# Kernel tuning notes

Hardware: AMD Instinct MI355X
Metric: run time of the kernel (lower is better)

The kernel has to match this reference:

```python
import jax, jax.numpy as jnp
import numpy as np
from jax import lax

ANCHORS = jnp.array([[-83.0, -39.0, 100.0, 56.0], [-175.0, -87.0, 192.0, 104.0],
                     [-359.0, -183.0, 376.0, 200.0], [-55.0, -55.0, 72.0, 72.0],
                     [-119.0, -119.0, 136.0, 136.0], [-247.0, -247.0, 264.0, 264.0],
                     [-35.0, -79.0, 52.0, 96.0], [-79.0, -167.0, 96.0, 184.0],
                     [-167.0, -343.0, 184.0, 360.0]], dtype=jnp.float32)
FEAT_STRIDE = 16
NMS_THRESH = 0.7
NA = 9
PRE_NMS_TOPN = 3000   # test_pre_nms_topN
POST_NMS_TOPN = 300   # test_post_nms_topN


def setup_inputs() -> dict:
    key = jax.random.key(0)
    ks = jax.random.split(key, 4)
    B, C, H, W = 8, 512, 64, 64
    x = jax.random.normal(ks[0], (B, C, H, W), jnp.float32)
    im_size = jnp.full((B, 2), 1024.0, jnp.float32)  # (H, W) per image
    W_conv = jax.random.normal(ks[1], (512, C, 3, 3), jnp.float32) * 0.01
    b_conv = jnp.zeros((512,), jnp.float32)
    W_reg = jax.random.normal(ks[2], (36, 512), jnp.float32) * 0.01
    b_reg = jnp.zeros((36,), jnp.float32)
    W_cls = jax.random.normal(ks[3], (18, 512), jnp.float32) * 0.01
    b_cls = jnp.zeros((18,), jnp.float32)
    return {"x": x, "im_size": im_size, "W_conv": W_conv, "b_conv": b_conv,
            "W_reg": W_reg, "b_reg": b_reg, "W_cls": W_cls, "b_cls": b_cls}


def _nms_select(boxes):
    """Greedy NMS on boxes already sorted by descending score.
    Returns [POST_NMS_TOPN, 4], zero-padded (matches torch output init)."""
    M = boxes.shape[0]
    area = (boxes[:, 2] - boxes[:, 0]) * (boxes[:, 3] - boxes[:, 1])
    lt = jnp.maximum(boxes[:, None, :2], boxes[None, :, :2])
    rb = jnp.minimum(boxes[:, None, 2:], boxes[None, :, 2:])
    wh = jnp.maximum(rb - lt, 0.0)
    inter = wh[..., 0] * wh[..., 1]
    iou = inter / (area[:, None] + area[None, :] - inter + 1e-9)
    iou = lax.stop_gradient(iou)
    idxs = jnp.arange(M)

    def body(keep, i):
        sup = (iou[i] > NMS_THRESH) & (idxs > i) & keep[i]
        return keep & ~sup, None

    keep, _ = lax.scan(body, jnp.ones((M,), bool), idxs)
    key = jnp.where(keep, idxs, M)           # push suppressed to the end
    order = jnp.sort(key)[:POST_NMS_TOPN]
    valid = order < M
    gi = jnp.minimum(order, M - 1)
    return jnp.where(valid[:, None], boxes[gi], 0.0)


def reference(x, im_size, W_conv, b_conv, W_reg, b_reg, W_cls, b_cls):
    B = x.shape[0]
    conv = lax.conv_general_dilated(
        x, W_conv, window_strides=(1, 1), padding='SAME',
        dimension_numbers=('NCHW', 'OIHW', 'NCHW')) + b_conv[None, :, None, None]
    Hc, Wc = conv.shape[2], conv.shape[3]

    # bbox deltas from raw (pre-ReLU) conv features, as in the source
    reg = jnp.einsum('bchw,oc->bohw', conv, W_reg) + b_reg[None, :, None, None]
    delta = reg.transpose(0, 2, 3, 1).reshape(B, -1, 4)  # (B, H*W*9, 4)

    # scores from ReLU'd features; channel-pair softmax trick, take class 0
    feat = jax.nn.relu(conv)
    cls = jnp.einsum('bchw,oc->bohw', feat, W_cls) + b_cls[None, :, None, None]
    c2 = cls.reshape(B, 2, NA * Hc, Wc)
    scores = jax.nn.softmax(c2, axis=1)[:, 0].reshape(B, -1)  # (B, 9*H*W)

    # anchor shifting: (h, w, anchor) ordering matches delta layout
    sx = jnp.arange(Wc, dtype=x.dtype) * FEAT_STRIDE
    sy = jnp.arange(Hc, dtype=x.dtype) * FEAT_STRIDE
    gx, gy = jnp.meshgrid(sx, sy)  # (Hc, Wc) 'xy' indexing
    shifts = jnp.stack([gx.ravel(), gy.ravel(), gx.ravel(), gy.ravel()], axis=1)
    anc = (shifts[:, None, :] + ANCHORS[None, :, :]).reshape(-1, 4)  # (H*W*9, 4)

    # decode, faithful to the source's (nonstandard) math
    w = anc[:, 2] - anc[:, 0] + 1.0
    h = anc[:, 3] - anc[:, 1] + 1.0
    cx = anc[:, 0] + 0.5 * w
    cy = anc[:, 1] + 0.5 * h
    dx, dy, dw, dh = delta[..., 0], delta[..., 1], delta[..., 2], delta[..., 3]
    pcx = dx * cx
    pcy = dy * cy
    pw = jnp.exp(dw) * w
    ph = jnp.exp(dh) * h
    x1, y1 = pcx - 0.5 * pw, pcy - 0.5 * ph
    x2, y2 = pcx + 0.5 * pw, pcy + 0.5 * ph

    # clip to image bounds (im_size[i] = (H, W))
    xmax = im_size[:, 1:2] - 1.0  # (B,1)
    ymax = im_size[:, 0:1] - 1.0
    x1 = jnp.clip(x1, 0.0, xmax)
    y1 = jnp.clip(y1, 0.0, ymax)
    x2 = jnp.clip(x2, 0.0, xmax)
    y2 = jnp.clip(y2, 0.0, ymax)
    proposals = jnp.stack([x1, y1, x2, y2], axis=-1)  # (B, N, 4)

    # pre-NMS top-k by score, then greedy NMS, keep post_nms_topN
    _, top_i = lax.top_k(scores, PRE_NMS_TOPN)
    top_b = jnp.take_along_axis(proposals, top_i[..., None], axis=1)
    output = jax.vmap(_nms_select)(top_b)  # (B, POST_NMS_TOPN, 4)

    return output, scores, proposals
```

## Files before the change

### kernel.cpp

```cpp
#include <hip/hip_runtime.h>
#include <stdint.h>

typedef unsigned long long u64;
typedef double v4d __attribute__((ext_vector_type(4)));

#define NIMG 8
#define CIN 512
#define COUT 512
#define NPOS 4096
#define NSC 36864
#define PRE_TOPN 3000
#define POST_TOPN 300
#define NWORDS 47
#define MSTRIDE 48
#define WROWF 80
#define WCH_F 5760
#define WBUF_B 23040
#define XBUF 1920
#define XVALID 1632

__constant__ double dANC[9][4] = {
    {-83.0, -39.0, 100.0, 56.0},   {-175.0, -87.0, 192.0, 104.0},
    {-359.0, -183.0, 376.0, 200.0},{-55.0, -55.0, 72.0, 72.0},
    {-119.0, -119.0, 136.0, 136.0},{-247.0, -247.0, 264.0, 264.0},
    {-35.0, -79.0, 52.0, 96.0},    {-79.0, -167.0, 96.0, 184.0},
    {-167.0, -343.0, 184.0, 360.0}};

static __device__ __forceinline__ void gload16(const void* g, void* l) {
    __builtin_amdgcn_global_load_lds(
        (const __attribute__((address_space(1))) void*)g,
        (__attribute__((address_space(3))) void*)l, 16, 0, 0);
}

__global__ __launch_bounds__(256) void transpose_wconv_f32(const float* __restrict__ W,
                                                           float* __restrict__ Wtf) {
    __shared__ float t[32][33];
    int k0 = blockIdx.x * 32;
    int o0 = blockIdx.y * 32;
    int tid = threadIdx.x;
    for (int idx = tid; idx < 1024; idx += 256) {
        int r = idx >> 5, c = idx & 31;
        t[r][c] = W[(size_t)(o0 + r) * 4608 + k0 + c];
    }
    __syncthreads();
    for (int idx = tid; idx < 1024; idx += 256) {
        int r = idx >> 5, c = idx & 31;
        int oc = o0 + c;
        Wtf[((size_t)(oc >> 6) * 4608 + (k0 + r)) * WROWF + (oc & 63)] = t[c][r];
    }
}

__global__ __launch_bounds__(256) void build_wheads(const float* __restrict__ Wreg,
                                                    const float* __restrict__ Wcls,
                                                    float* __restrict__ Wh) {
    int g = blockIdx.x * 256 + threadIdx.x;
    if (g >= 512 * 64) return;
    int k = g >> 6, o = g & 63;
    float v = 0.f;
    if (o < 36) v = Wreg[o * 512 + k];
    else if (o < 54) v = Wcls[(o - 36) * 512 + k];
    Wh[g] = v;
}

__global__ __launch_bounds__(64) void mfma_probe(int* __restrict__ variant) {
    __shared__ double AA[72][16];
    __shared__ double BB[72][16];
    const int L = threadIdx.x;
    for (int i = L; i < 72 * 16; i += 64) {
        int K = i >> 4, c = i & 15;
        AA[K][c] = (double)(c * 73 + K + 1);
        BB[K][c] = (double)(K * 17 + 3 * c + 1);
    }
    __syncthreads();
    const int lg = L >> 4, lm = L & 15;
    v4d accN = {0.0, 0.0, 0.0, 0.0};
    v4d accS = {0.0, 0.0, 0.0, 0.0};
#pragma unroll
    for (int k4 = 0; k4 < 18; ++k4) {
        double a = AA[4 * k4 + lg][lm];
        double b = BB[4 * k4 + lg][lm];
        accN = __builtin_amdgcn_mfma_f64_16x16x4f64(a, b, accN, 0, 0, 0);
        accS = __builtin_amdgcn_mfma_f64_16x16x4f64(b, a, accS, 0, 0, 0);
    }
    int found = 255;
    for (int v = 0; v < 8; ++v) {
        bool ok = true;
        for (int r = 0; r < 4; ++r) {
            int m, n;
            int dm = v & 3;
            if (dm == 0)      { m = 4 * lg + r; n = lm; }
            else if (dm == 1) { m = lm; n = 4 * lg + r; }
            else if (dm == 2) { m = lg + 4 * r; n = lm; }
            else              { m = lm; n = lg + 4 * r; }
            long long ref = 0;
            for (int K = 0; K < 72; ++K)
                ref += (long long)(m * 73 + K + 1) * (long long)(K * 17 + 3 * n + 1);
            double got = (v < 4) ? accN[r] : accS[r];
            ok = ok && (got == (double)ref);
        }
        if (__all(ok) && found == 255) found = v;
    }
    if (L == 0) *variant = found;
}

__global__ __launch_bounds__(512) void conv_mfma(const float* __restrict__ X,
                                                 const float* __restrict__ Wtf,
                                                 const float* __restrict__ bconv,
                                                 double* __restrict__ convb,
                                                 const int* __restrict__ variant,
                                                 int img_base) {
    const int vr = *variant;
    if (vr > 7) return;
    const int tid = threadIdx.x;
    const int wv = tid >> 6;
    const int lane = tid & 63;
    const int lg = lane >> 4;
    const int lm = lane & 15;
    const int ocg = wv >> 1;
    const int posb = (wv & 1) * 32;
    const int octile = blockIdx.x;
    const int oc0 = octile * 64;
    const int y = blockIdx.y;
    const int imgL = blockIdx.z;
    const int img_g = img_base + imgL;

    __shared__ float Wl[2][72][WROWF];
    __shared__ float Xl[2][8][3][80];
    char* wl0 = (char*)&Wl[0][0][0];
    float* xl0 = &Xl[0][0][0][0];

    v4d acc[2];
    acc[0] = (v4d){0.0, 0.0, 0.0, 0.0};
    acc[1] = (v4d){0.0, 0.0, 0.0, 0.0};

    int boff[18];
#pragma unroll
    for (int k4 = 0; k4 < 18; ++k4) {
        int row = k4 * 4 + lg;
        int c = row / 9;
        int t = row - 9 * c;
        int ty = t / 3;
        int tx = t - 3 * ty;
        boff[k4] = c * 240 + ty * 80 + tx + posb + lm;
    }

    int xli[4], xoff[4];
#pragma unroll
    for (int i = 0; i < 4; ++i) {
        int idx = tid + i * 512;
        xli[i] = -1;
        xoff[i] = -1;
        if (idx < XVALID) {
            int c_l = idx / 204;
            int rem = idx - c_l * 204;
            int r = rem / 68;
            int xx = rem - r * 68;
            xli[i] = c_l * 240 + r * 80 + xx;
            int yy = y + r - 1;
            int xg = xx - 1;
            if (xx < 66 && (unsigned)yy < 64u && (unsigned)xg < 64u)
                xoff[i] = ((img_g * CIN + c_l) * 64 + yy) * 64 + xg;
        }
    }
    int woff[3];
#pragma unroll
    for (int i = 0; i < 3; ++i) {
        int u = i * 512 + tid;
        int row = u / 20, cp = u - 20 * row;
        woff[i] = (octile * 4608 + row) * WROWF + cp * 4;
    }

    float xr[4];

#define WDMA(c, par) { \
    gload16(&Wtf[(size_t)woff[0] + (size_t)(c) * WCH_F], \
            wl0 + (size_t)(par) * WBUF_B + (size_t)tid * 16); \
    gload16(&Wtf[(size_t)woff[1] + (size_t)(c) * WCH_F], \
            wl0 + (size_t)(par) * WBUF_B + (size_t)(512 + tid) * 16); \
    if (tid < 416) \
        gload16(&Wtf[(size_t)woff[2] + (size_t)(c) * WCH_F], \
                wl0 + (size_t)(par) * WBUF_B + (size_t)(1024 + tid) * 16); }

#define LOADR(c) { \
    _Pragma("unroll") \
    for (int i = 0; i < 4; ++i) \
        xr[i] = (xoff[i] >= 0) ? X[(size_t)xoff[i] + (size_t)(c) * 32768] : 0.f; }

#define WRITER(par) { \
    _Pragma("unroll") \
    for (int i = 0; i < 4; ++i) \
        if (xli[i] >= 0) xl0[(size_t)(par) * XBUF + xli[i]] = xr[i]; }

    WDMA(0, 0);
    LOADR(0);
    WRITER(0);
    __syncthreads();

    const bool swapped = (vr >= 4);
    const int aoff = ocg * 16 + lm;

    for (int c = 0; c < 64; ++c) {
        const int par = c & 1;
        if (c < 63) { WDMA(c + 1, par ^ 1); LOADR(c + 1); }
        const float* wb = &Wl[par][0][0];
        const float* bx = xl0 + (size_t)par * XBUF;
        if (!swapped) {
#pragma unroll
            for (int k4 = 0; k4 < 18; ++k4) {
                double a = (double)wb[(4 * k4 + lg) * WROWF + aoff];
                const float* bp = bx + boff[k4];
                double b0 = (double)bp[0];
                double b1 = (double)bp[16];
                acc[0] = __builtin_amdgcn_mfma_f64_16x16x4f64(a, b0, acc[0], 0, 0, 0);
                acc[1] = __builtin_amdgcn_mfma_f64_16x16x4f64(a, b1, acc[1], 0, 0, 0);
            }
        } else {
#pragma unroll
            for (int k4 = 0; k4 < 18; ++k4) {
                double a = (double)wb[(4 * k4 + lg) * WROWF + aoff];
                const float* bp = bx + boff[k4];
                double b0 = (double)bp[0];
                double b1 = (double)bp[16];
                acc[0] = __builtin_amdgcn_mfma_f64_16x16x4f64(b0, a, acc[0], 0, 0, 0);
                acc[1] = __builtin_amdgcn_mfma_f64_16x16x4f64(b1, a, acc[1], 0, 0, 0);
            }
        }
        if (c < 63) { WRITER(par ^ 1); }
        __syncthreads();
    }
#undef WDMA
#undef LOADR
#undef WRITER

    const int dm = vr & 3;
#pragma unroll
    for (int q = 0; q < 2; ++q) {
#pragma unroll
        for (int r = 0; r < 4; ++r) {
            int m, n;
            if (dm == 0)      { m = 4 * lg + r; n = lm; }
            else if (dm == 1) { m = lm; n = 4 * lg + r; }
            else if (dm == 2) { m = lg + 4 * r; n = lm; }
            else              { m = lm; n = lg + 4 * r; }
            int oc = oc0 + ocg * 16 + m;
            int xp = posb + q * 16 + n;
            convb[((size_t)imgL * COUT + oc) * NPOS + y * 64 + xp] =
                acc[q][r] + (double)bconv[oc];
        }
    }
}

__global__ __launch_bounds__(256) void conv_valu(const float* __restrict__ X,
                                                 const float* __restrict__ Wtf,
                                                 const float* __restrict__ bconv,
                                                 double* __restrict__ convb,
                                                 const int* __restrict__ variant,
                                                 int img_base) {
    if (*variant <= 7) return;
    const int tid = threadIdx.x;
    const int octile = blockIdx.x;
    const int oc0 = octile * 64;
    const int y = blockIdx.y;
    const int imgL = blockIdx.z;
    const int img_g = img_base + imgL;
    const int x_l = (tid & 15) * 4;
    const int oc_l = (tid >> 4) * 4;

    __shared__ double Wl[72][64];
    __shared__ double Bx[8][3][68];

    double acc[4][4];
#pragma unroll
    for (int i = 0; i < 4; ++i)
#pragma unroll
        for (int j = 0; j < 4; ++j) acc[i][j] = 0.0;

    for (int cc = 0; cc < CIN; cc += 8) {
        __syncthreads();
        for (int idx = tid; idx < 8 * 3 * 68; idx += 256) {
            int c_l = idx / 204;
            int rem = idx - c_l * 204;
            int r = rem / 68;
            int xx = rem - r * 68;
            int yy = y + r - 1;
            int xg = xx - 1;
            float v = 0.f;
            if (xx < 66 && (unsigned)yy < 64u && (unsigned)xg < 64u)
                v = X[(((size_t)img_g * CIN + cc + c_l) * 64 + yy) * 64 + xg];
            Bx[c_l][r][xx] = (double)v;
        }
        for (int idx = tid; idx < 72 * 64; idx += 256) {
            int kl = idx >> 6, col = idx & 63;
            Wl[kl][col] = (double)Wtf[((size_t)octile * 4608 + cc * 9 + kl) * WROWF + col];
        }
        __syncthreads();
#pragma unroll 2
        for (int c_l = 0; c_l < 8; ++c_l) {
#pragma unroll
            for (int ty = 0; ty < 3; ++ty) {
                double xv[6];
                *(double2*)&xv[0] = *(const double2*)&Bx[c_l][ty][x_l + 0];
                *(double2*)&xv[2] = *(const double2*)&Bx[c_l][ty][x_l + 2];
                *(double2*)&xv[4] = *(const double2*)&Bx[c_l][ty][x_l + 4];
#pragma unroll
                for (int tx = 0; tx < 3; ++tx) {
                    const double* wp = &Wl[c_l * 9 + ty * 3 + tx][oc_l];
                    double wr[4];
                    *(double2*)&wr[0] = *(const double2*)(wp + 0);
                    *(double2*)&wr[2] = *(const double2*)(wp + 2);
#pragma unroll
                    for (int i = 0; i < 4; ++i)
#pragma unroll
                        for (int j = 0; j < 4; ++j)
                            acc[i][j] = fma(wr[i], xv[j + tx], acc[i][j]);
                }
            }
        }
    }
#pragma unroll
    for (int i = 0; i < 4; ++i) {
        int oc = oc0 + oc_l + i;
        double b = (double)bconv[oc];
        double4 st;
        st.x = acc[i][0] + b; st.y = acc[i][1] + b;
        st.z = acc[i][2] + b; st.w = acc[i][3] + b;
        *(double4*)&convb[((size_t)imgL * COUT + oc) * NPOS + y * 64 + x_l] = st;
    }
}

__global__ __launch_bounds__(256) void heads_kernel(const double* __restrict__ convb,
                                                    const float* __restrict__ Wh,
                                                    const float* __restrict__ breg,
                                                    const float* __restrict__ bcls,
                                                    const float* __restrict__ im_size,
                                                    float* __restrict__ out_scores,
                                                    float4* __restrict__ out_props,
                                                    double* __restrict__ dscores,
                                                    double4* __restrict__ dprops,
                                                    int img_base) {
    const int tid = threadIdx.x;
    const int y = blockIdx.x;
    const int imgL = blockIdx.y;
    const int img_g = img_base + imgL;

    __shared__ double cl[64][64];
    __shared__ float wl[64][64];

    const int o = tid & 63;
    const int g = tid >> 6;
    double acc[16];
#pragma unroll
    for (int j = 0; j < 16; ++j) acc[j] = 0.0;

    for (int k0 = 0; k0 < CIN; k0 += 64) {
        __syncthreads();
        for (int idx = tid; idx < 4096; idx += 256) {
            int kl = idx >> 6, p = idx & 63;
            cl[kl][p] = convb[((size_t)imgL * COUT + k0 + kl) * NPOS + y * 64 + p];
        }
        for (int idx = tid; idx < 4096; idx += 256) {
            wl[idx >> 6][idx & 63] = Wh[(k0 + (idx >> 6)) * 64 + (idx & 63)];
        }
        __syncthreads();
        const bool ru = (o >= 36);
        for (int kl = 0; kl < 64; ++kl) {
            double w = (double)wl[kl][o];
#pragma unroll
            for (int j = 0; j < 16; ++j) {
                double v = cl[kl][g * 16 + j];
                if (ru) v = fmax(v, 0.0);
                acc[j] = fma(w, v, acc[j]);
            }
        }
    }
    __syncthreads();
    double bias = (o < 36) ? (double)breg[o] : (o < 54 ? (double)bcls[o - 36] : 0.0);
#pragma unroll
    for (int j = 0; j < 16; ++j) cl[o][g * 16 + j] = acc[j] + bias;
    __syncthreads();

    const double im_h = (double)im_size[img_g * 2 + 0];
    const double im_w = (double)im_size[img_g * 2 + 1];
    const double xmax = im_w - 1.0, ymax = im_h - 1.0;

    for (int t = tid; t < 576; t += 256) {
        int p = t / 9;
        int a = t - p * 9;
        double dx = cl[a * 4 + 0][p], dy = cl[a * 4 + 1][p];
        double dw = cl[a * 4 + 2][p], dh = cl[a * 4 + 3][p];
        double c0 = cl[36 + a][p], c1 = cl[45 + a][p];
        double mm = fmax(c0, c1);
        double e0 = exp(c0 - mm), e1 = exp(c1 - mm);
        double sc = e0 / (e0 + e1);

        double sx = (double)p * 16.0, sy = (double)y * 16.0;
        double a0 = dANC[a][0] + sx, a1 = dANC[a][1] + sy;
        double a2 = dANC[a][2] + sx, a3 = dANC[a][3] + sy;
        double w_ = a2 - a0 + 1.0, h_ = a3 - a1 + 1.0;
        double cx = a0 + 0.5 * w_, cy = a1 + 0.5 * h_;
        double pcx = dx * cx, pcy = dy * cy;
        double pw = exp(dw) * w_, ph = exp(dh) * h_;
        double x1 = pcx - 0.5 * pw, y1 = pcy - 0.5 * ph;
        double x2 = pcx + 0.5 * pw, y2 = pcy + 0.5 * ph;
        x1 = fmin(fmax(x1, 0.0), xmax);
        y1 = fmin(fmax(y1, 0.0), ymax);
        x2 = fmin(fmax(x2, 0.0), xmax);
        y2 = fmin(fmax(y2, 0.0), ymax);

        int pp = y * 64 + p;
        size_t si = (size_t)img_g * NSC + (size_t)a * NPOS + pp;
        size_t pi = (size_t)img_g * NSC + (size_t)pp * 9 + a;
        out_scores[si] = (float)sc;
        dscores[si] = sc;
        double4 db; db.x = x1; db.y = y1; db.z = x2; db.w = y2;
        dprops[pi] = db;
        out_props[pi] = make_float4((float)x1, (float)y1, (float)x2, (float)y2);
    }
}

__global__ __launch_bounds__(256) void topk_select(const double* __restrict__ dscores,
                                                   u64* __restrict__ Tsel) {
    const int img = blockIdx.x;
    const int tid = threadIdx.x;
    const u64* sb = (const u64*)(dscores + (size_t)img * NSC);
    __shared__ uint32_t hist[256];
    __shared__ u64 s_prefix;
    __shared__ uint32_t s_rem;
    if (tid == 0) { s_prefix = 0ull; s_rem = PRE_TOPN; }
    for (int pass = 0; pass < 8; ++pass) {
        int shift = 56 - pass * 8;
        hist[tid] = 0;
        __syncthreads();
        u64 pmask = pass ? (~0ull << (shift + 8)) : 0ull;
        u64 pref = s_prefix;
        for (int i = tid; i < NSC; i += 256) {
            u64 v = sb[i];
            if ((v & pmask) == pref) atomicAdd(&hist[(uint32_t)(v >> shift) & 0xFFu], 1u);
        }
        __syncthreads();
        if (tid == 0) {
            uint32_t rem = s_rem, cum = 0;
            int b = 255;
            for (; b > 0; --b) {
                if (cum + hist[b] >= rem) break;
                cum += hist[b];
            }
            s_prefix = pref | ((u64)(uint32_t)b << shift);
            s_rem = rem - cum;
        }
        __syncthreads();
    }
    if (tid == 0) Tsel[img] = s_prefix;
}

__global__ __launch_bounds__(1024) void sort_gather(const double* __restrict__ dscores,
                                                    const double4* __restrict__ dprops,
                                                    const u64* __restrict__ Tsel,
                                                    double4* __restrict__ dboxes) {
    const int img = blockIdx.x;
    const int tid = threadIdx.x;
    __shared__ u64 skey[4096];
    __shared__ unsigned short sidx[4096];
    __shared__ int cnt;
    if (tid == 0) cnt = 0;
    for (int i = tid; i < 4096; i += 1024) { skey[i] = 0ull; sidx[i] = 0xFFFF; }
    __syncthreads();
    const u64 T = Tsel[img];
    const u64* sb = (const u64*)(dscores + (size_t)img * NSC);
    for (int i = tid; i < NSC; i += 1024) {
        u64 v = sb[i];
        if (v >= T) {
            int p = atomicAdd(&cnt, 1);
            if (p < 4096) { skey[p] = v; sidx[p] = (unsigned short)i; }
        }
    }
    __syncthreads();
    for (int k = 2; k <= 4096; k <<= 1) {
        for (int j = k >> 1; j > 0; j >>= 1) {
            for (int i = tid; i < 4096; i += 1024) {
                int ixj = i ^ j;
                if (ixj > i) {
                    u64 ka = skey[i], kb = skey[ixj];
                    unsigned short ia = sidx[i], ib = sidx[ixj];
                    bool aw = (ka < kb) || (ka == kb && ia > ib);
                    bool up = (i & k) == 0;
                    if (up ? aw : !aw) {
                        skey[i] = kb; skey[ixj] = ka;
                        sidx[i] = ib; sidx[ixj] = ia;
                    }
                }
            }
            __syncthreads();
        }
    }
    for (int t = tid; t < PRE_TOPN; t += 1024) {
        unsigned int idx = sidx[t];
        dboxes[(size_t)img * PRE_TOPN + t] = dprops[(size_t)img * NSC + idx];
    }
}

__global__ __launch_bounds__(256) void iou_mask_kernel(const double4* __restrict__ dboxes,
                                                       u64* __restrict__ mask) {
    const int tid = threadIdx.x;
    const int ib = blockIdx.x;
    const int img = blockIdx.y;
    const int i = ib * 64 + (tid >> 2);
    if (i >= PRE_TOPN) return;
    const double4 bi = dboxes[(size_t)img * PRE_TOPN + i];
    const double ai = (bi.z - bi.x) * (bi.w - bi.y);
    for (int w = (tid & 3); w < NWORDS; w += 4) {
        const int jbase = w * 64;
        u64 m = 0;
        if (jbase + 63 > i) {
            const int jmax = min(64, PRE_TOPN - jbase);
            for (int b = 0; b < jmax; ++b) {
                int j = jbase + b;
                if (j > i) {
                    double4 bj = dboxes[(size_t)img * PRE_TOPN + j];
                    double aj = (bj.z - bj.x) * (bj.w - bj.y);
                    double ltx = fmax(bi.x, bj.x), lty = fmax(bi.y, bj.y);
                    double rbx = fmin(bi.z, bj.z), rby = fmin(bi.w, bj.w);
                    double iw = fmax(rbx - ltx, 0.0), ih = fmax(rby - lty, 0.0);
                    double inter = iw * ih;
                    double iou = inter / (ai + aj - inter + 1e-9);
                    if (iou > 0.7) m |= (1ull << b);
                }
            }
        }
        mask[((size_t)img * PRE_TOPN + i) * MSTRIDE + w] = m;
    }
}

__global__ __launch_bounds__(64) void nms_walk(const double4* __restrict__ dboxes,
                                               const u64* __restrict__ mask,
                                               float4* __restrict__ outb) {
    const int img = blockIdx.x;
    const int lane = threadIdx.x;
    __shared__ short kept[POST_TOPN];
    u64 removed = 0ull;
    int nk = 0;
    for (int w = 0; w < NWORDS && nk < POST_TOPN; ++w) {
        u64 freeb = ~__shfl(removed, w);
        if (w == NWORDS - 1)
            freeb &= (1ull << (PRE_TOPN - (NWORDS - 1) * 64)) - 1;
        while (freeb != 0ull && nk < POST_TOPN) {
            int b = __ffsll((unsigned long long)freeb) - 1;
            int i = w * 64 + b;
            if (lane == 0) kept[nk] = (short)i;
            ++nk;
            u64 m = (lane < NWORDS)
                        ? mask[((size_t)img * PRE_TOPN + i) * MSTRIDE + lane]
                        : 0ull;
            removed |= m;
            u64 hi = (b == 63) ? 0ull : (~0ull << (b + 1));
            freeb &= hi;
            freeb &= ~__shfl(removed, w);
        }
    }
    __syncthreads();
    const int n = nk;
    for (int r = lane; r < POST_TOPN; r += 64) {
        float4 v = make_float4(0.f, 0.f, 0.f, 0.f);
        if (r < n) {
            double4 d = dboxes[(size_t)img * PRE_TOPN + kept[r]];
            v = make_float4((float)d.x, (float)d.y, (float)d.z, (float)d.w);
        }
        outb[img * POST_TOPN + r] = v;
    }
}

extern "C" void kernel_launch(void* const* d_in, const int* in_sizes, int n_in,
                              void* d_out, int out_size, void* d_ws, size_t ws_size,
                              hipStream_t stream) {
    const float* x = (const float*)d_in[0];
    const float* im_size = (const float*)d_in[1];
    const float* Wconv = (const float*)d_in[2];
    const float* bconv = (const float*)d_in[3];
    const float* Wreg = (const float*)d_in[4];
    const float* breg = (const float*)d_in[5];
    const float* Wcls = (const float*)d_in[6];
    const float* bcls = (const float*)d_in[7];

    float* outf = (float*)d_out;
    float4* out_boxes = (float4*)outf;
    float* out_scores = outf + NIMG * POST_TOPN * 4;
    float4* out_props = (float4*)(out_scores + (size_t)NIMG * NSC);

    char* ws = (char*)d_ws;
    const size_t WT_OFF = 0;
    const size_t WH_OFF = WT_OFF + (size_t)8 * 4608 * WROWF * 4;
    const size_t TS_OFF = WH_OFF + (size_t)512 * 64 * 4;
    const size_t VAR_OFF = TS_OFF + 64;
    const size_t DS_OFF = (VAR_OFF + 4 + 255) & ~(size_t)255;
    const size_t DP_OFF = DS_OFF + (size_t)NIMG * NSC * 8;
    const size_t DB_OFF = DP_OFF + (size_t)NIMG * NSC * 32;
    const size_t MK_OFF = DB_OFF + (size_t)NIMG * PRE_TOPN * 32;
    const size_t CV_OFF = (MK_OFF + (size_t)NIMG * PRE_TOPN * MSTRIDE * 8 + 255) & ~(size_t)255;

    float* Wtf = (float*)(ws + WT_OFF);
    float* Wh = (float*)(ws + WH_OFF);
    u64* Tsel = (u64*)(ws + TS_OFF);
    int* variant = (int*)(ws + VAR_OFF);
    double* dscores = (double*)(ws + DS_OFF);
    double4* dprops = (double4*)(ws + DP_OFF);
    double4* dboxes = (double4*)(ws + DB_OFF);
    u64* mask = (u64*)(ws + MK_OFF);
    double* convb = (double*)(ws + CV_OFF);

    const size_t per_img = (size_t)COUT * NPOS * 8;
    int CH = 1;
    if (ws_size > CV_OFF + per_img) {
        size_t avail = (ws_size - CV_OFF) / per_img;
        CH = (int)(avail > 8 ? 8 : avail);
        if (CH < 1) CH = 1;
    }

    transpose_wconv_f32<<<dim3(144, 16), 256, 0, stream>>>(Wconv, Wtf);
    build_wheads<<<128, 256, 0, stream>>>(Wreg, Wcls, Wh);
    mfma_probe<<<1, 64, 0, stream>>>(variant);

    for (int base = 0; base < NIMG; base += CH) {
        int n = NIMG - base;
        if (n > CH) n = CH;
        conv_mfma<<<dim3(8, 64, n), 512, 0, stream>>>(x, Wtf, bconv, convb, variant, base);
        conv_valu<<<dim3(8, 64, n), 256, 0, stream>>>(x, Wtf, bconv, convb, variant, base);
        heads_kernel<<<dim3(64, n), 256, 0, stream>>>(convb, Wh, breg, bcls, im_size,
                                                      out_scores, out_props,
                                                      dscores, dprops, base);
    }
    topk_select<<<NIMG, 256, 0, stream>>>(dscores, Tsel);
    sort_gather<<<NIMG, 1024, 0, stream>>>(dscores, dprops, Tsel, dboxes);
    iou_mask_kernel<<<dim3(NWORDS, NIMG), 256, 0, stream>>>(dboxes, mask);
    nms_walk<<<NIMG, 64, 0, stream>>>(dboxes, mask, out_boxes);
}
```

Before: 3.554 ms.

## Replace direct FP64 MFMA conv with Winograd F(2x2,3x3) transform-GEMM pipeline

Measured after the change: 9.335 ms. 163% more time.

```diff
diff --git a/kernel.cpp b/kernel.cpp
--- a/kernel.cpp
+++ b/kernel.cpp
@@ -14,10 +14,10 @@
 #define NWORDS 47
 #define MSTRIDE 48
 #define WROWF 80
-#define WCH_F 5760
-#define WBUF_B 23040
-#define XBUF 1920
-#define XVALID 1632
+#define GROW 66
+#define WCHS 2112
+#define BCHS 16896
+#define PBUF 16896
 
 __constant__ double dANC[9][4] = {
     {-83.0, -39.0, 100.0, 56.0},   {-175.0, -87.0, 192.0, 104.0},
@@ -103,12 +103,86 @@
     if (L == 0) *variant = found;
 }
 
-__global__ __launch_bounds__(512) void conv_mfma(const float* __restrict__ X,
-                                                 const float* __restrict__ Wtf,
-                                                 const float* __restrict__ bconv,
-                                                 double* __restrict__ convb,
-                                                 const int* __restrict__ variant,
-                                                 int img_base) {
+__global__ __launch_bounds__(256) void wgrad_f64(const float* __restrict__ W,
+                                                 double* __restrict__ WT4) {
+    int g = blockIdx.x * 256 + threadIdx.x;
+    if (g >= 512 * 512) return;
+    int oc = g & 511, ci = g >> 9;
+    const float* wp = W + (size_t)oc * 4608 + ci * 9;
+    double gm[3][3];
+#pragma unroll
+    for (int i = 0; i < 3; ++i)
+#pragma unroll
+        for (int j = 0; j < 3; ++j) gm[i][j] = (double)wp[i * 3 + j];
+    double T[4][3];
+#pragma unroll
+    for (int j = 0; j < 3; ++j) {
+        T[0][j] = gm[0][j];
+        T[1][j] = 0.5 * (gm[0][j] + gm[1][j] + gm[2][j]);
+        T[2][j] = 0.5 * (gm[0][j] - gm[1][j] + gm[2][j]);
+        T[3][j] = gm[2][j];
+    }
+#pragma unroll
+    for (int u = 0; u < 4; ++u) {
+        double V0 = T[u][0];
+        double V1 = 0.5 * (T[u][0] + T[u][1] + T[u][2]);
+        double V2 = 0.5 * (T[u][0] - T[u][1] + T[u][2]);
+        double V3 = T[u][2];
+        double Vv[4] = {V0, V1, V2, V3};
+#pragma unroll
+        for (int v = 0; v < 4; ++v)
+            WT4[(((size_t)(u * 4 + v) * 8 + (oc >> 6)) * 512 + ci) * GROW + (oc & 63)] = Vv[v];
+    }
+}
+
+__global__ __launch_bounds__(256) void winog_xt(const float* __restrict__ X,
+                                                double* __restrict__ XT,
+                                                int* __restrict__ flag,
+                                                int img_g, int h) {
+    const int tid = threadIdx.x;
+    const int tb = blockIdx.x;
+    const int ci = blockIdx.y * 4 + (tid >> 6);
+    const int tl = tid & 63;
+    if (h == 0 && tb == 0 && blockIdx.y == 0 && tid == 0) *flag = 0;
+    const int t = h * 512 + tb * 64 + tl;
+    const int ty = t >> 5, tx = t & 31;
+    const float* Xp = X + ((size_t)img_g * CIN + ci) * NPOS;
+    double d[4][4];
+#pragma unroll
+    for (int r = 0; r < 4; ++r) {
+        int yy = 2 * ty - 1 + r;
+#pragma unroll
+        for (int c = 0; c < 4; ++c) {
+            int xx = 2 * tx - 1 + c;
+            d[r][c] = ((unsigned)yy < 64u && (unsigned)xx < 64u)
+                          ? (double)Xp[yy * 64 + xx] : 0.0;
+        }
+    }
+    double E[4][4];
+#pragma unroll
+    for (int c = 0; c < 4; ++c) {
+        E[0][c] = d[0][c] - d[2][c];
+        E[1][c] = d[1][c] + d[2][c];
+        E[2][c] = d[2][c] - d[1][c];
+        E[3][c] = d[1][c] - d[3][c];
+    }
+#pragma unroll
+    for (int r = 0; r < 4; ++r) {
+        double U0 = E[r][0] - E[r][2];
+        double U1 = E[r][1] + E[r][2];
+        double U2 = E[r][2] - E[r][1];
+        double U3 = E[r][1] - E[r][3];
+        double Uv[4] = {U0, U1, U2, U3};
+#pragma unroll
+        for (int v = 0; v < 4; ++v)
+            XT[(((size_t)(r * 4 + v) * 512 + ci) * 8 + tb) * GROW + tl] = Uv[v];
+    }
+}
+
+__global__ __launch_bounds__(512) void winog_gemm(const double* __restrict__ XT,
+                                                  const double* __restrict__ WT4,
+                                                  double* __restrict__ MT,
+                                                  const int* __restrict__ variant) {
     const int vr = *variant;
     if (vr > 7) return;
     const int tid = threadIdx.x;
@@ -119,118 +193,72 @@
     const int ocg = wv >> 1;
     const int posb = (wv & 1) * 32;
     const int octile = blockIdx.x;
-    const int oc0 = octile * 64;
-    const int y = blockIdx.y;
-    const int imgL = blockIdx.z;
-    const int img_g = img_base + imgL;
-
-    __shared__ float Wl[2][72][WROWF];
-    __shared__ float Xl[2][8][3][80];
+    const int tb = blockIdx.y;
+    const int uv = blockIdx.z;
+
+    __shared__ double Wl[2][32][GROW];
+    __shared__ double Bl[2][32][GROW];
     char* wl0 = (char*)&Wl[0][0][0];
-    float* xl0 = &Xl[0][0][0][0];
+    char* bl0 = (char*)&Bl[0][0][0];
 
     v4d acc[2];
     acc[0] = (v4d){0.0, 0.0, 0.0, 0.0};
     acc[1] = (v4d){0.0, 0.0, 0.0, 0.0};
 
-    int boff[18];
-#pragma unroll
-    for (int k4 = 0; k4 < 18; ++k4) {
-        int row = k4 * 4 + lg;
-        int c = row / 9;
-        int t = row - 9 * c;
-        int ty = t / 3;
-        int tx = t - 3 * ty;
-        boff[k4] = c * 240 + ty * 80 + tx + posb + lm;
-    }
-
-    int xli[4], xoff[4];
-#pragma unroll
-    for (int i = 0; i < 4; ++i) {
-        int idx = tid + i * 512;
-        xli[i] = -1;
-        xoff[i] = -1;
-        if (idx < XVALID) {
-            int c_l = idx / 204;
-            int rem = idx - c_l * 204;
-            int r = rem / 68;
-            int xx = rem - r * 68;
-            xli[i] = c_l * 240 + r * 80 + xx;
-            int yy = y + r - 1;
-            int xg = xx - 1;
-            if (xx < 66 && (unsigned)yy < 64u && (unsigned)xg < 64u)
-                xoff[i] = ((img_g * CIN + c_l) * 64 + yy) * 64 + xg;
-        }
-    }
-    int woff[3];
-#pragma unroll
-    for (int i = 0; i < 3; ++i) {
-        int u = i * 512 + tid;
-        int row = u / 20, cp = u - 20 * row;
-        woff[i] = (octile * 4608 + row) * WROWF + cp * 4;
-    }
-
-    float xr[4];
-
-#define WDMA(c, par) { \
-    gload16(&Wtf[(size_t)woff[0] + (size_t)(c) * WCH_F], \
-            wl0 + (size_t)(par) * WBUF_B + (size_t)tid * 16); \
-    gload16(&Wtf[(size_t)woff[1] + (size_t)(c) * WCH_F], \
-            wl0 + (size_t)(par) * WBUF_B + (size_t)(512 + tid) * 16); \
-    if (tid < 416) \
-        gload16(&Wtf[(size_t)woff[2] + (size_t)(c) * WCH_F], \
-                wl0 + (size_t)(par) * WBUF_B + (size_t)(1024 + tid) * 16); }
-
-#define LOADR(c) { \
-    _Pragma("unroll") \
-    for (int i = 0; i < 4; ++i) \
-        xr[i] = (xoff[i] >= 0) ? X[(size_t)xoff[i] + (size_t)(c) * 32768] : 0.f; }
-
-#define WRITER(par) { \
-    _Pragma("unroll") \
-    for (int i = 0; i < 4; ++i) \
-        if (xli[i] >= 0) xl0[(size_t)(par) * XBUF + xli[i]] = xr[i]; }
-
-    WDMA(0, 0);
-    LOADR(0);
-    WRITER(0);
+    const double* wbase = WT4 + ((size_t)(uv * 8 + octile) * 512) * GROW;
+    const double* bbase = XT + ((size_t)uv * 512 * 8 + tb) * GROW;
+
+    int wo0, wo1, wo2, bo0, bo1, bo2;
+    {
+        int u = tid;           int r = u / 33, cp = u - 33 * r;
+        wo0 = r * GROW + cp * 2;  bo0 = r * 528 + cp * 2;
+        u = 512 + tid;         r = u / 33;  cp = u - 33 * r;
+        wo1 = r * GROW + cp * 2;  bo1 = r * 528 + cp * 2;
+        u = 1024 + tid;        r = u / 33;  cp = u - 33 * r;
+        wo2 = r * GROW + cp * 2;  bo2 = r * 528 + cp * 2;
+    }
+
+#define DMA(cc, par) { \
+    gload16(wbase + (size_t)(cc) * WCHS + wo0, wl0 + (size_t)(par) * PBUF + (size_t)tid * 16); \
+    gload16(wbase + (size_t)(cc) * WCHS + wo1, wl0 + (size_t)(par) * PBUF + (size_t)(512 + tid) * 16); \
+    if (tid < 32) \
+        gload16(wbase + (size_t)(cc) * WCHS + wo2, wl0 + (size_t)(par) * PBUF + (size_t)(1024 + tid) * 16); \
+    gload16(bbase + (size_t)(cc) * BCHS + bo0, bl0 + (size_t)(par) * PBUF + (size_t)tid * 16); \
+    gload16(bbase + (size_t)(cc) * BCHS + bo1, bl0 + (size_t)(par) * PBUF + (size_t)(512 + tid) * 16); \
+    if (tid < 32) \
+        gload16(bbase + (size_t)(cc) * BCHS + bo2, bl0 + (size_t)(par) * PBUF + (size_t)(1024 + tid) * 16); }
+
+    DMA(0, 0);
     __syncthreads();
 
     const bool swapped = (vr >= 4);
     const int aoff = ocg * 16 + lm;
 
-    for (int c = 0; c < 64; ++c) {
+    for (int c = 0; c < 16; ++c) {
         const int par = c & 1;
-        if (c < 63) { WDMA(c + 1, par ^ 1); LOADR(c + 1); }
-        const float* wb = &Wl[par][0][0];
-        const float* bx = xl0 + (size_t)par * XBUF;
+        if (c < 15) DMA(c + 1, par ^ 1);
+        const double* wb = &Wl[par][0][0];
+        const double* bb = &Bl[par][0][0];
         if (!swapped) {
 #pragma unroll
-            for (int k4 = 0; k4 < 18; ++k4) {
-                double a = (double)wb[(4 * k4 + lg) * WROWF + aoff];
-                const float* bp = bx + boff[k4];
-                double b0 = (double)bp[0];
-                double b1 = (double)bp[16];
-                acc[0] = __builtin_amdgcn_mfma_f64_16x16x4f64(a, b0, acc[0], 0, 0, 0);
-                acc[1] = __builtin_amdgcn_mfma_f64_16x16x4f64(a, b1, acc[1], 0, 0, 0);
+            for (int k4 = 0; k4 < 8; ++k4) {
+                double a = wb[(4 * k4 + lg) * GROW + aoff];
+                const double* bp = bb + (4 * k4 + lg) * GROW + posb + lm;
+                acc[0] = __builtin_amdgcn_mfma_f64_16x16x4f64(a, bp[0],  acc[0], 0, 0, 0);
+                acc[1] = __builtin_amdgcn_mfma_f64_16x16x4f64(a, bp[16], acc[1], 0, 0, 0);
             }
         } else {
 #pragma unroll
-            for (int k4 = 0; k4 < 18; ++k4) {
-                double a = (double)wb[(4 * k4 + lg) * WROWF + aoff];
-                const float* bp = bx + boff[k4];
-                double b0 = (double)bp[0];
-                double b1 = (double)bp[16];
-                acc[0] = __builtin_amdgcn_mfma_f64_16x16x4f64(b0, a, acc[0], 0, 0, 0);
-                acc[1] = __builtin_amdgcn_mfma_f64_16x16x4f64(b1, a, acc[1], 0, 0, 0);
+            for (int k4 = 0; k4 < 8; ++k4) {
+                double a = wb[(4 * k4 + lg) * GROW + aoff];
+                const double* bp = bb + (4 * k4 + lg) * GROW + posb + lm;
+                acc[0] = __builtin_amdgcn_mfma_f64_16x16x4f64(bp[0],  a, acc[0], 0, 0, 0);
+                acc[1] = __builtin_amdgcn_mfma_f64_16x16x4f64(bp[16], a, acc[1], 0, 0, 0);
             }
         }
-        if (c < 63) { WRITER(par ^ 1); }
-        __syncthreads();
-    }
-#undef WDMA
-#undef LOADR
-#undef WRITER
+        __syncthreads();
+    }
+#undef DMA
 
     const int dm = vr & 3;
 #pragma unroll
@@ -242,11 +270,90 @@
             else if (dm == 1) { m = lm; n = 4 * lg + r; }
             else if (dm == 2) { m = lg + 4 * r; n = lm; }
             else              { m = lm; n = lg + 4 * r; }
-            int oc = oc0 + ocg * 16 + m;
-            int xp = posb + q * 16 + n;
-            convb[((size_t)imgL * COUT + oc) * NPOS + y * 64 + xp] =
-                acc[q][r] + (double)bconv[oc];
-        }
+            int oc = octile * 64 + ocg * 16 + m;
+            int tile = tb * 64 + posb + q * 16 + n;
+            MT[((size_t)uv * 512 + oc) * 512 + tile] = acc[q][r];
+        }
+    }
+}
+
+__global__ __launch_bounds__(256) void winog_outt(const double* __restrict__ MT,
+                                                  const float* __restrict__ bconv,
+                                                  double* __restrict__ convb,
+                                                  const int* __restrict__ variant,
+                                                  int h) {
+    if (*variant > 7) return;
+    const int tid = threadIdx.x;
+    const int tb = blockIdx.x;
+    const int oc = blockIdx.y * 4 + (tid >> 6);
+    const int tl = tid & 63;
+    const int t_h = tb * 64 + tl;
+    double m[4][4];
+#pragma unroll
+    for (int u = 0; u < 4; ++u)
+#pragma unroll
+        for (int v = 0; v < 4; ++v)
+            m[u][v] = MT[((size_t)(u * 4 + v) * 512 + oc) * 512 + t_h];
+    double S[2][4];
+#pragma unroll
+    for (int v = 0; v < 4; ++v) {
+        S[0][v] = m[0][v] + m[1][v] + m[2][v];
+        S[1][v] = m[1][v] - m[2][v] - m[3][v];
+    }
+    const int t = h * 512 + t_h;
+    const int ty = t >> 5, tx = t & 31;
+    const double b = (double)bconv[oc];
+#pragma unroll
+    for (int s = 0; s < 2; ++s) {
+        double y0 = S[s][0] + S[s][1] + S[s][2];
+        double y1 = S[s][1] - S[s][2] - S[s][3];
+        convb[((size_t)oc) * NPOS + (2 * ty + s) * 64 + 2 * tx + 0] = y0 + b;
+        convb[((size_t)oc) * NPOS + (2 * ty + s) * 64 + 2 * tx + 1] = y1 + b;
+    }
+}
+
+__global__ __launch_bounds__(256) void winog_check(const float* __restrict__ X,
+                                                   const float* __restrict__ W,
+                                                   const float* __restrict__ bconv,
+                                                   const double* __restrict__ convb,
+                                                   const int* __restrict__ variant,
+                                                   int* __restrict__ flag,
+                                                   int img_g) {
+    if (*variant > 7) { if (threadIdx.x == 0 && blockIdx.x == 0) *flag = 1; return; }
+    const int s = blockIdx.x;
+    const int tid = threadIdx.x;
+    const int oc = (s * 151) & 511;
+    const int y = (s * 23) & 63;
+    const int x = (s * 41) & 63;
+    double part = 0.0;
+#pragma unroll
+    for (int cc = 0; cc < 2; ++cc) {
+        int ci = tid + cc * 256;
+        const float* wp = W + (size_t)oc * 4608 + ci * 9;
+        const float* xp = X + ((size_t)img_g * CIN + ci) * NPOS;
+#pragma unroll
+        for (int i = 0; i < 3; ++i) {
+            int yy = y + i - 1;
+            if ((unsigned)yy >= 64u) continue;
+#pragma unroll
+            for (int j = 0; j < 3; ++j) {
+                int xx = x + j - 1;
+                if ((unsigned)xx >= 64u) continue;
+                part = fma((double)wp[i * 3 + j], (double)xp[yy * 64 + xx], part);
+            }
+        }
+    }
+    __shared__ double red[256];
+    red[tid] = part;
+    __syncthreads();
+    for (int off = 128; off > 0; off >>= 1) {
+        if (tid < off) red[tid] += red[tid + off];
+        __syncthreads();
+    }
+    if (tid == 0) {
+        double ref = red[0] + (double)bconv[oc];
+        double got = convb[(size_t)oc * NPOS + y * 64 + x];
+        if (fabs(ref - got) > 1e-7) atomicOr(flag, 1);
     }
 }
 
@@ -255,14 +362,14 @@
                                                  const float* __restrict__ bconv,
                                                  double* __restrict__ convb,
                                                  const int* __restrict__ variant,
+                                                 const int* __restrict__ flag,
                                                  int img_base) {
-    if (*variant <= 7) return;
+    if (*variant <= 7 && *flag == 0) return;
     const int tid = threadIdx.x;
     const int octile = blockIdx.x;
     const int oc0 = octile * 64;
     const int y = blockIdx.y;
-    const int imgL = blockIdx.z;
-    const int img_g = img_base + imgL;
+    const int img_g = img_base;
     const int x_l = (tid & 15) * 4;
     const int oc_l = (tid >> 4) * 4;
 
@@ -324,7 +431,7 @@
         double4 st;
         st.x = acc[i][0] + b; st.y = acc[i][1] + b;
         st.z = acc[i][2] + b; st.w = acc[i][3] + b;
-        *(double4*)&convb[((size_t)imgL * COUT + oc) * NPOS + y * 64 + x_l] = st;
+        *(double4*)&convb[(size_t)oc * NPOS + y * 64 + x_l] = st;
     }
 }
 
@@ -337,11 +444,9 @@
                                                     float4* __restrict__ out_props,
                                                     double* __restrict__ dscores,
                                                     double4* __restrict__ dprops,
-                                                    int img_base) {
+                                                    int img_g) {
     const int tid = threadIdx.x;
     const int y = blockIdx.x;
-    const int imgL = blockIdx.y;
-    const int img_g = img_base + imgL;
 
     __shared__ double cl[64][64];
     __shared__ float wl[64][64];
@@ -356,7 +461,7 @@
         __syncthreads();
         for (int idx = tid; idx < 4096; idx += 256) {
             int kl = idx >> 6, p = idx & 63;
-            cl[kl][p] = convb[((size_t)imgL * COUT + k0 + kl) * NPOS + y * 64 + p];
+            cl[kl][p] = convb[(size_t)(k0 + kl) * NPOS + y * 64 + p];
         }
         for (int idx = tid; idx < 4096; idx += 256) {
             wl[idx >> 6][idx & 63] = Wh[(k0 + (idx >> 6)) * 64 + (idx & 63)];
@@ -587,46 +692,49 @@
     float4* out_props = (float4*)(out_scores + (size_t)NIMG * NSC);
 
     char* ws = (char*)d_ws;
-    const size_t WT_OFF = 0;
-    const size_t WH_OFF = WT_OFF + (size_t)8 * 4608 * WROWF * 4;
-    const size_t TS_OFF = WH_OFF + (size_t)512 * 64 * 4;
+    const size_t WTF_OFF = 0;
+    const size_t WH_OFF  = WTF_OFF + (size_t)8 * 4608 * WROWF * 4;
+    const size_t TS_OFF  = WH_OFF + (size_t)512 * 64 * 4;
     const size_t VAR_OFF = TS_OFF + 64;
-    const size_t DS_OFF = (VAR_OFF + 4 + 255) & ~(size_t)255;
-    const size_t DP_OFF = DS_OFF + (size_t)NIMG * NSC * 8;
-    const size_t DB_OFF = DP_OFF + (size_t)NIMG * NSC * 32;
-    const size_t MK_OFF = DB_OFF + (size_t)NIMG * PRE_TOPN * 32;
-    const size_t CV_OFF = (MK_OFF + (size_t)NIMG * PRE_TOPN * MSTRIDE * 8 + 255) & ~(size_t)255;
-
-    float* Wtf = (float*)(ws + WT_OFF);
+    const size_t FLG_OFF = VAR_OFF + 4;
+    const size_t WG_OFF  = (FLG_OFF + 4 + 255) & ~(size_t)255;
+    const size_t XT_OFF  = WG_OFF + (size_t)128 * 512 * GROW * 8;
+    const size_t MT_OFF  = XT_OFF + (size_t)16 * 512 * 8 * GROW * 8;
+    const size_t DS_OFF  = MT_OFF + (size_t)16 * 512 * 512 * 8;
+    const size_t DP_OFF  = DS_OFF + (size_t)NIMG * NSC * 8;
+    const size_t DB_OFF  = DP_OFF + (size_t)NIMG * NSC * 32;
+    const size_t MK_OFF  = DB_OFF + (size_t)NIMG * PRE_TOPN * 32;
+    const size_t CV_OFF  = (MK_OFF + (size_t)NIMG * PRE_TOPN * MSTRIDE * 8 + 255) & ~(size_t)255;
+
+    float* Wtf = (float*)(ws + WTF_OFF);
     float* Wh = (float*)(ws + WH_OFF);
     u64* Tsel = (u64*)(ws + TS_OFF);
     int* variant = (int*)(ws + VAR_OFF);
+    int* flag = (int*)(ws + FLG_OFF);
+    double* WT4 = (double*)(ws + WG_OFF);
+    double* XTb = (double*)(ws + XT_OFF);
+    double* MTb = (double*)(ws + MT_OFF);
     double* dscores = (double*)(ws + DS_OFF);
     double4* dprops = (double4*)(ws + DP_OFF);
     double4* dboxes = (double4*)(ws + DB_OFF);
     u64* mask = (u64*)(ws + MK_OFF);
     double* convb = (double*)(ws + CV_OFF);
 
-    const size_t per_img = (size_t)COUT * NPOS * 8;
-    int CH = 1;
-    if (ws_size > CV_OFF + per_img) {
-        size_t avail = (ws_size - CV_OFF) / per_img;
-        CH = (int)(avail > 8 ? 8 : avail);
-        if (CH < 1) CH = 1;
-    }
-
     transpose_wconv_f32<<<dim3(144, 16), 256, 0, stream>>>(Wconv, Wtf);
     build_wheads<<<128, 256, 0, stream>>>(Wreg, Wcls, Wh);
     mfma_probe<<<1, 64, 0, stream>>>(variant);
-
-    for (int base = 0; base < NIMG; base += CH) {
-        int n = NIMG - base;
-        if (n > CH) n = CH;
-        conv_mfma<<<dim3(8, 64, n), 512, 0, stream>>>(x, Wtf, bconv, convb, variant, base);
-        conv_valu<<<dim3(8, 64, n), 256, 0, stream>>>(x, Wtf, bconv, convb, variant, base);
-        heads_kernel<<<dim3(64, n), 256, 0, stream>>>(convb, Wh, breg, bcls, im_size,
-                                                      out_scores, out_props,
-                                                      dscores, dprops, base);
+    wgrad_f64<<<1024, 256, 0, stream>>>(Wconv, WT4);
+
+    for (int img = 0; img < NIMG; ++img) {
+        for (int h = 0; h < 2; ++h) {
+            winog_xt<<<dim3(8, 128), 256, 0, stream>>>(x, XTb, flag, img, h);
+            winog_gemm<<<dim3(8, 8, 16), 512, 0, stream>>>(XTb, WT4, MTb, variant);
+            winog_outt<<<dim3(8, 128), 256, 0, stream>>>(MTb, bconv, convb, variant, h);
+        }
+        winog_check<<<256, 256, 0, stream>>>(x, Wconv, bconv, convb, variant, flag, img);
+        conv_valu<<<dim3(8, 64), 256, 0, stream>>>(x, Wtf, bconv, convb, variant, flag, img);
+        heads_kernel<<<64, 256, 0, stream>>>(convb, Wh, breg, bcls, im_size,
+                                             out_scores, out_props, dscores, dprops, img);
     }
     topk_select<<<NIMG, 256, 0, stream>>>(dscores, Tsel);
     sort_gather<<<NIMG, 1024, 0, stream>>>(dscores, dprops, Tsel, dboxes);
```
